# Kernel optimization log

Measured on AMD Instinct MI355X. Metric: run time of the kernel, lower is better.

Reference implementation:

```python
import jax, jax.numpy as jnp
import numpy as np

B, NOISE, HID, EMB, VOCAB, T = 256, 64, 256, 128, 32000, 16
PAD_ID = 0
TAU = 1.0
EPS = 1e-10


def setup_inputs() -> dict:
    key = jax.random.key(0)
    ks = jax.random.split(key, 11)
    s = 0.02
    return {
        "noise": jax.random.normal(ks[0], (B, NOISE), jnp.float32),
        "gumbel_u": jax.random.uniform(ks[1], (T, B, VOCAB), jnp.float32),
        "fc_W": jax.random.normal(ks[2], (HID, NOISE), jnp.float32) * s,
        "fc_b": jnp.zeros((HID,), jnp.float32),
        "embed_W": jax.random.normal(ks[3], (VOCAB, EMB), jnp.float32) * s,
        "W_ih": jax.random.normal(ks[4], (4 * HID, EMB), jnp.float32) * s,
        "W_hh": jax.random.normal(ks[5], (4 * HID, HID), jnp.float32) * s,
        "b_ih": jnp.zeros((4 * HID,), jnp.float32),
        "b_hh": jnp.zeros((4 * HID,), jnp.float32),
        "out_W": jax.random.normal(ks[6], (VOCAB, HID), jnp.float32) * s,
        "out_b": jnp.zeros((VOCAB,), jnp.float32),
    }


def reference(noise, gumbel_u, fc_W, fc_b, embed_W, W_ih, W_hh, b_ih, b_hh, out_W, out_b):
    # h0 = tanh(fc(noise)); c0 = 0; first input = embed(<PAD>)
    h0 = jnp.tanh(noise @ fc_W.T + fc_b)                       # [B, HID]
    c0 = jnp.zeros_like(h0)
    x0 = jnp.broadcast_to(embed_W[PAD_ID], (noise.shape[0], embed_W.shape[1]))

    def step(carry, g_u):
        h, c, x = carry
        gates = x @ W_ih.T + b_ih + h @ W_hh.T + b_hh           # [B, 4H]
        i_g, f_g, g_g, o_g = jnp.split(gates, 4, axis=-1)
        i_g = jax.nn.sigmoid(i_g)
        f_g = jax.nn.sigmoid(f_g)
        g_g = jnp.tanh(g_g)
        o_g = jax.nn.sigmoid(o_g)
        c = f_g * c + i_g * g_g
        h = o_g * jnp.tanh(c)
        logits = h @ out_W.T + out_b                            # [B, V]
        gumbel = -jnp.log(-jnp.log(g_u + EPS) + EPS)
        y_soft = jax.nn.softmax((logits + gumbel) / TAU, axis=-1)
        idx = jnp.argmax(y_soft, axis=-1)                       # [B]
        y_hard = jax.nn.one_hot(idx, logits.shape[-1], dtype=y_soft.dtype)
        token = y_hard - jax.lax.stop_gradient(y_soft) + y_soft  # straight-through
        x_next = embed_W[idx]                                   # [B, EMB]
        return (h, c, x_next), token

    _, tokens = jax.lax.scan(step, (h0, c0, x0), gumbel_u)      # [T, B, V]
    return jnp.transpose(tokens, (1, 0, 2))                     # [B, T, V]
```

## Files before the change

### kernel.cpp

```cpp
#include <hip/hip_runtime.h>
#include <math.h>

#define NB 256
#define NH 256
#define NE 128
#define NV 32000
#define TT 16
#define NZ 64

#define MAXC 192
#define UTHR 0.9979f
#define GNC  6.17f

__device__ __forceinline__ unsigned fkey(float f) {
    unsigned u = __float_as_uint(f);
    return (u & 0x80000000u) ? ~u : (u | 0x80000000u);
}
__device__ __forceinline__ float unfkey(unsigned k) {
    return __uint_as_float((k & 0x80000000u) ? (k & 0x7fffffffu) : ~k);
}
__device__ __forceinline__ unsigned long long sx64(unsigned long long v, int m) {
    unsigned lo = (unsigned)__shfl_xor((int)(unsigned)(v & 0xffffffffull), m, 64);
    unsigned hi = (unsigned)__shfl_xor((int)(unsigned)(v >> 32), m, 64);
    return ((unsigned long long)hi << 32) | (unsigned long long)lo;
}

__global__ void k_init(const float* __restrict__ noise, const float* __restrict__ fcW,
                       const float* __restrict__ fcb, float* __restrict__ h,
                       float* __restrict__ c, unsigned* __restrict__ maxWnU) {
    __shared__ float ns[NZ];
    int b = blockIdx.x, tid = threadIdx.x;
    if (tid < NZ) ns[tid] = noise[b * NZ + tid];
    __syncthreads();
    float acc = fcb[tid];
    const float* w = &fcW[(size_t)tid * NZ];
#pragma unroll
    for (int k = 0; k < NZ; k++) acc += ns[k] * w[k];
    h[b * NH + tid] = tanhf(acc);
    c[b * NH + tid] = 0.f;
    if (b == 0 && tid == 0) *maxWnU = 0u;
}

__global__ __launch_bounds__(256) void k_wnorm(const float* __restrict__ W,
                                               unsigned* __restrict__ maxWnU) {
    int lane = threadIdx.x & 63;
    int wv = blockIdx.x * 4 + (threadIdx.x >> 6);
    float best = 0.f;
    for (int r = wv * 64; r < wv * 64 + 64; r++) {
        const float* row = &W[(size_t)r * NH];
        float p = 0.f;
#pragma unroll
        for (int q = 0; q < 4; q++) {
            float x = row[lane + 64 * q];
            p += x * x;
        }
#pragma unroll
        for (int m = 1; m <= 32; m <<= 1) p += __shfl_xor(p, m, 64);
        best = fmaxf(best, p);
    }
    if (lane == 0) atomicMax(maxWnU, __float_as_uint(sqrtf(best) * 1.0001f + 1e-6f));
}

__global__ __launch_bounds__(256) void k_prep(const float* __restrict__ gu,
                                              float* __restrict__ out,
                                              int* __restrict__ counts,
                                              float2* __restrict__ cands) {
    __shared__ int cnt;
    __shared__ float2 lc[MAXC];
    int r = blockIdx.x;
    int t = r >> 8, b = r & 255;
    int tid = threadIdx.x;
    if (tid == 0) cnt = 0;
    __syncthreads();
    const float4* g4 = (const float4*)gu + (size_t)r * (NV / 4);
    float4* o4 = (float4*)out + ((size_t)b * TT + t) * (NV / 4);
    float4 z = make_float4(0.f, 0.f, 0.f, 0.f);
    for (int i = tid; i < NV / 4; i += 256) {
        float4 u = g4[i];
        o4[i] = z;
        float uv[4] = {u.x, u.y, u.z, u.w};
#pragma unroll
        for (int comp = 0; comp < 4; comp++) {
            if (uv[comp] > UTHR) {
                int k = atomicAdd(&cnt, 1);
                if (k < MAXC) {
                    float gm = -logf(-logf(uv[comp] + 1e-10f) + 1e-10f);
                    lc[k] = make_float2(gm, __int_as_float(i * 4 + comp));
                }
            }
        }
    }
    __syncthreads();
    int n = cnt > MAXC ? MAXC : cnt;
    if (tid == 0) counts[r] = cnt;
    if (tid < n) cands[(size_t)r * MAXC + tid] = lc[tid];
}

__global__ __launch_bounds__(256) void k_gates(
    const float* __restrict__ h, const float* __restrict__ embW,
    const float* __restrict__ Wih, const float* __restrict__ Whh,
    const float* __restrict__ bih, const float* __restrict__ bhh,
    float* __restrict__ gates, const int* __restrict__ idxPrev, int t) {
    __shared__ float As[16][68];
    __shared__ float Ws[16][68];
    __shared__ int idxs[64];
    int tid = threadIdx.x;
    int n0 = blockIdx.x * 64, m0 = blockIdx.y * 64;
    if (tid < 64) {
        idxs[tid] = (t == 0) ? 0 : idxPrev[m0 + tid];
    }
    float acc[4][4] = {};
    int row = tid >> 2, kq = tid & 3;
    int ty = tid >> 4, tx = tid & 15;
    for (int kc = 0; kc < 24; kc++) {
        __syncthreads();
        int kg = kc * 16 + kq * 4;
        float4 a4, w4;
        if (kg < NE) {
            a4 = *(const float4*)&embW[(size_t)idxs[row] * NE + kg];
            w4 = *(const float4*)&Wih[(size_t)(n0 + row) * NE + kg];
        } else {
            a4 = *(const float4*)&h[(size_t)(m0 + row) * NH + kg - NE];
            w4 = *(const float4*)&Whh[(size_t)(n0 + row) * NH + kg - NE];
        }
        As[kq * 4 + 0][row] = a4.x; As[kq * 4 + 1][row] = a4.y;
        As[kq * 4 + 2][row] = a4.z; As[kq * 4 + 3][row] = a4.w;
        Ws[kq * 4 + 0][row] = w4.x; Ws[kq * 4 + 1][row] = w4.y;
        Ws[kq * 4 + 2][row] = w4.z; Ws[kq * 4 + 3][row] = w4.w;
        __syncthreads();
#pragma unroll
        for (int kk = 0; kk < 16; kk++) {
            float a[4], w[4];
            *(float4*)&a[0] = *(const float4*)&As[kk][ty * 4];
            *(float4*)&w[0] = *(const float4*)&Ws[kk][tx * 4];
#pragma unroll
            for (int i = 0; i < 4; i++)
#pragma unroll
                for (int j = 0; j < 4; j++) acc[i][j] += a[i] * w[j];
        }
    }
#pragma unroll
    for (int i = 0; i < 4; i++) {
        int b = m0 + ty * 4 + i;
#pragma unroll
        for (int j = 0; j < 4; j++) {
            int n = n0 + tx * 4 + j;
            gates[(size_t)b * (4 * NH) + n] = acc[i][j] + bih[n] + bhh[n];
        }
    }
}

__global__ __launch_bounds__(256) void k_cellcand(
    const float* __restrict__ gates, float* __restrict__ c, float* __restrict__ h,
    const int* __restrict__ counts, const float2* __restrict__ cands,
    const float* __restrict__ W, const float* __restrict__ outb,
    const float* __restrict__ gu, const unsigned* __restrict__ maxWnU,
    int* __restrict__ idxs, float* __restrict__ out, int t) {
    __shared__ float hsh[NH];
    __shared__ float hred[4];
    __shared__ unsigned long long bks[4];
    __shared__ int fbflag;
    int b = blockIdx.x, tid = threadIdx.x;
    int lane = tid & 63, w = tid >> 6;

    const float* g = &gates[(size_t)b * (4 * NH)];
    float ig = g[tid], fg = g[NH + tid], gg = g[2 * NH + tid], og = g[3 * NH + tid];
    float is = 1.f / (1.f + expf(-ig));
    float fs = 1.f / (1.f + expf(-fg));
    float gt = tanhf(gg);
    float os = 1.f / (1.f + expf(-og));
    float cn = fs * c[b * NH + tid] + is * gt;
    c[b * NH + tid] = cn;
    float hv = os * tanhf(cn);
    h[b * NH + tid] = hv;
    hsh[tid] = hv;
    float p = hv * hv;
#pragma unroll
    for (int m = 1; m <= 32; m <<= 1) p += __shfl_xor(p, m, 64);
    if (lane == 0) hred[w] = p;
    __syncthreads();

    int r = t * NB + b;
    int nc = counts[r];
    unsigned long long bk = 0;
    if (nc >= 1 && nc <= MAXC) {
        const float2* cr = &cands[(size_t)r * MAXC];
        for (int ci = w; ci < nc; ci += 4) {
            float2 cd = cr[ci];
            int v = __float_as_int(cd.y);
            const float* Wr = &W[(size_t)v * NH];
            float d = 0.f;
#pragma unroll
            for (int q = 0; q < 4; q++) d += hsh[lane + 64 * q] * Wr[lane + 64 * q];
#pragma unroll
            for (int m = 1; m <= 32; m <<= 1) d += __shfl_xor(d, m, 64);
            float s = d + outb[v] + cd.x;
            unsigned long long key =
                ((unsigned long long)fkey(s) << 32) | (unsigned)(NV - 1 - v);
            if (key > bk) bk = key;
        }
    }
    if (lane == 0) bks[w] = bk;
    __syncthreads();
    if (tid == 0) {
        unsigned long long k = bks[0];
        for (int q = 1; q < 4; q++)
            if (bks[q] > k) k = bks[q];
        bks[0] = k;
        float hh2 = hred[0] + hred[1] + hred[2] + hred[3];
        float D = sqrtf(hh2) * 1.0001f * __uint_as_float(*maxWnU) + 0.01f;
        float bs = unfkey((unsigned)(k >> 32));
        fbflag = (nc < 1 || nc > MAXC || !(bs >= GNC + D)) ? 1 : 0;
    }
    __syncthreads();
    if (fbflag) {
        const float* gur = &gu[((size_t)t * NB + b) * NV];
        unsigned long long fk = 0;
        for (int v = tid; v < NV; v += 256) {
            float uv = gur[v];
            float gm = -logf(-logf(uv + 1e-10f) + 1e-10f);
            const float* Wr = &W[(size_t)v * NH];
            float d = 0.f;
            for (int k2 = 0; k2 < NH; k2++) d += hsh[k2] * Wr[k2];
            float s = d + outb[v] + gm;
            unsigned long long key =
                ((unsigned long long)fkey(s) << 32) | (unsigned)(NV - 1 - v);
            if (key > fk) fk = key;
        }
#pragma unroll
        for (int m = 1; m <= 32; m <<= 1) {
            unsigned long long o = sx64(fk, m);
            if (o > fk) fk = o;
        }
        if (lane == 0) bks[w] = fk;
        __syncthreads();
        if (tid == 0) {
            unsigned long long k = bks[0];
            for (int q = 1; q < 4; q++)
                if (bks[q] > k) k = bks[q];
            bks[0] = k;
        }
        __syncthreads();
    }
    if (tid == 0) {
        unsigned long long k = bks[0];
        int v = NV - 1 - (int)(unsigned)(k & 0xffffffffu);
        idxs[t * NB + b] = v;
        out[((size_t)b * TT + t) * NV + v] = 1.0f;
    }
}

extern "C" void kernel_launch(void* const* d_in, const int* in_sizes, int n_in,
                              void* d_out, int out_size, void* d_ws, size_t ws_size,
                              hipStream_t stream) {
    const float* noise = (const float*)d_in[0];
    const float* gu    = (const float*)d_in[1];
    const float* fcW   = (const float*)d_in[2];
    const float* fcb   = (const float*)d_in[3];
    const float* embW  = (const float*)d_in[4];
    const float* Wih   = (const float*)d_in[5];
    const float* Whh   = (const float*)d_in[6];
    const float* bih   = (const float*)d_in[7];
    const float* bhh   = (const float*)d_in[8];
    const float* outW  = (const float*)d_in[9];
    const float* outb  = (const float*)d_in[10];
    float* out = (float*)d_out;

    float* ws = (float*)d_ws;
    float* h      = ws;
    float* c      = ws + 65536;
    float* gates  = ws + 131072;
    int* idxs     = (int*)(ws + 393216);
    int* counts   = (int*)(ws + 397312);
    unsigned* maxWnU = (unsigned*)(ws + 401408);
    float2* cands = (float2*)(ws + 401416);

    k_init<<<NB, NH, 0, stream>>>(noise, fcW, fcb, h, c, maxWnU);
    k_wnorm<<<125, 256, 0, stream>>>(outW, maxWnU);
    k_prep<<<TT * NB, 256, 0, stream>>>(gu, out, counts, cands);

    for (int t = 0; t < TT; t++) {
        const int* idxPrev = idxs + (t > 0 ? (t - 1) * NB : 0);
        k_gates<<<dim3(16, 4), 256, 0, stream>>>(h, embW, Wih, Whh, bih, bhh, gates,
                                                 idxPrev, t);
        k_cellcand<<<NB, 256, 0, stream>>>(gates, c, h, counts, cands, outW, outb, gu,
                                           maxWnU, idxs, out, t);
    }
}
```

Baseline: 1.897 ms.

## Fuse LSTM timestep loop into one persistent kernel with packed gate weights

Replaces the per-timestep gate GEMM and cell/candidate kernels with a single kernel. Each block keeps the state of 4 batch rows in registers and shared memory across all 16 steps, using input and hidden weights pre-packed into a gate-interleaved float4 layout. Candidate logit evaluation is double-buffered over 8 candidates, and the output bias is folded into the precomputed Gumbel values. This removes 32 launches and the global round-trips for gates, h, c and idx. In exchange only 64 blocks run, every block rereads the full packed weight matrix each step, and the full-vocabulary fallback now runs on a single wave per row.

```diff
diff --git a/kernel.cpp b/kernel.cpp
--- a/kernel.cpp
+++ b/kernel.cpp
@@ -12,6 +12,8 @@
 #define UTHR 0.9979f
 #define GNC  6.17f
 
+typedef __attribute__((ext_vector_type(4))) float f32x4;
+
 __device__ __forceinline__ unsigned fkey(float f) {
     unsigned u = __float_as_uint(f);
     return (u & 0x80000000u) ? ~u : (u | 0x80000000u);
@@ -25,24 +27,25 @@
     return ((unsigned long long)hi << 32) | (unsigned long long)lo;
 }
 
-__global__ void k_init(const float* __restrict__ noise, const float* __restrict__ fcW,
-                       const float* __restrict__ fcb, float* __restrict__ h,
-                       float* __restrict__ c, unsigned* __restrict__ maxWnU) {
-    __shared__ float ns[NZ];
-    int b = blockIdx.x, tid = threadIdx.x;
-    if (tid < NZ) ns[tid] = noise[b * NZ + tid];
-    __syncthreads();
-    float acc = fcb[tid];
-    const float* w = &fcW[(size_t)tid * NZ];
-#pragma unroll
-    for (int k = 0; k < NZ; k++) acc += ns[k] * w[k];
-    h[b * NH + tid] = tanhf(acc);
-    c[b * NH + tid] = 0.f;
-    if (b == 0 && tid == 0) *maxWnU = 0u;
+__global__ void k_pack(const float* __restrict__ Wih, const float* __restrict__ Whh,
+                       f32x4* __restrict__ Wp, unsigned* __restrict__ maxWnU,
+                       unsigned* __restrict__ maxObU) {
+    int k = blockIdx.x;
+    int j = threadIdx.x;
+    f32x4 v;
+#pragma unroll
+    for (int g = 0; g < 4; ++g) {
+        int n = (g << 8) + j;
+        ((float*)&v)[g] = (k < NE) ? Wih[(size_t)n * NE + k] : Whh[(size_t)n * NH + (k - NE)];
+    }
+    Wp[k * 256 + j] = v;
+    if (k == 0 && j == 0) { *maxWnU = 0u; *maxObU = 0u; }
 }
 
 __global__ __launch_bounds__(256) void k_wnorm(const float* __restrict__ W,
-                                               unsigned* __restrict__ maxWnU) {
+                                               const float* __restrict__ outb,
+                                               unsigned* __restrict__ maxWnU,
+                                               unsigned* __restrict__ maxObU) {
     int lane = threadIdx.x & 63;
     int wv = blockIdx.x * 4 + (threadIdx.x >> 6);
     float best = 0.f;
@@ -59,9 +62,14 @@
         best = fmaxf(best, p);
     }
     if (lane == 0) atomicMax(maxWnU, __float_as_uint(sqrtf(best) * 1.0001f + 1e-6f));
+    float ob = outb[blockIdx.x * 256 + threadIdx.x];
+#pragma unroll
+    for (int m = 1; m <= 32; m <<= 1) ob = fmaxf(ob, __shfl_xor(ob, m, 64));
+    if (lane == 0) atomicMax(maxObU, fkey(ob));
 }
 
 __global__ __launch_bounds__(256) void k_prep(const float* __restrict__ gu,
+                                              const float* __restrict__ outb,
                                               float* __restrict__ out,
                                               int* __restrict__ counts,
                                               float2* __restrict__ cands) {
@@ -84,8 +92,9 @@
             if (uv[comp] > UTHR) {
                 int k = atomicAdd(&cnt, 1);
                 if (k < MAXC) {
-                    float gm = -logf(-logf(uv[comp] + 1e-10f) + 1e-10f);
-                    lc[k] = make_float2(gm, __int_as_float(i * 4 + comp));
+                    int v = i * 4 + comp;
+                    float gm = -logf(-logf(uv[comp] + 1e-10f) + 1e-10f) + outb[v];
+                    lc[k] = make_float2(gm, __int_as_float(v));
                 }
             }
         }
@@ -96,157 +105,175 @@
     if (tid < n) cands[(size_t)r * MAXC + tid] = lc[tid];
 }
 
-__global__ __launch_bounds__(256) void k_gates(
-    const float* __restrict__ h, const float* __restrict__ embW,
-    const float* __restrict__ Wih, const float* __restrict__ Whh,
-    const float* __restrict__ bih, const float* __restrict__ bhh,
-    float* __restrict__ gates, const int* __restrict__ idxPrev, int t) {
-    __shared__ float As[16][68];
-    __shared__ float Ws[16][68];
-    __shared__ int idxs[64];
+struct Cand8 {
+    f32x4 w[8];
+    float g[8];
+    int v[8];
+};
+__device__ __forceinline__ void load8(Cand8& cb, const float2* __restrict__ cr, int base,
+                                      int nc, const float* __restrict__ W, int lane) {
+#pragma unroll
+    for (int i = 0; i < 8; ++i) {
+        int ci = base + i;
+        float2 cd = (ci < nc) ? cr[ci] : make_float2(-1e30f, __int_as_float(0));
+        int v = __float_as_int(cd.y);
+        cb.g[i] = cd.x;
+        cb.v[i] = v;
+        cb.w[i] = *(const f32x4*)&W[(size_t)v * NH + (lane << 2)];
+    }
+}
+__device__ __forceinline__ void comp8(const Cand8& cb, f32x4 hx, unsigned long long& bk) {
+#pragma unroll
+    for (int i = 0; i < 8; ++i) {
+        f32x4 pr = hx * cb.w[i];
+        float d = pr.x + pr.y + pr.z + pr.w;
+#pragma unroll
+        for (int m = 1; m <= 32; m <<= 1) d += __shfl_xor(d, m, 64);
+        float s = d + cb.g[i];
+        unsigned long long key =
+            ((unsigned long long)fkey(s) << 32) | (unsigned)(NV - 1 - cb.v[i]);
+        if (key > bk) bk = key;
+    }
+}
+
+__global__ __launch_bounds__(256) void k_main(
+    const float* __restrict__ noise, const float* __restrict__ fcW,
+    const float* __restrict__ fcb, const float* __restrict__ embW,
+    const f32x4* __restrict__ Wp, const float* __restrict__ bih,
+    const float* __restrict__ bhh, const int* __restrict__ counts,
+    const float2* __restrict__ cands, const float* __restrict__ W,
+    const float* __restrict__ outb, const float* __restrict__ gu,
+    const unsigned* __restrict__ maxWnU, const unsigned* __restrict__ maxObU,
+    float* __restrict__ out) {
+    __shared__ f32x4 xhp[384];
+    __shared__ float hrow[4][256];
+    __shared__ float ns[256];
     int tid = threadIdx.x;
-    int n0 = blockIdx.x * 64, m0 = blockIdx.y * 64;
-    if (tid < 64) {
-        idxs[tid] = (t == 0) ? 0 : idxPrev[m0 + tid];
-    }
-    float acc[4][4] = {};
-    int row = tid >> 2, kq = tid & 3;
-    int ty = tid >> 4, tx = tid & 15;
-    for (int kc = 0; kc < 24; kc++) {
+    int lane = tid & 63, w = tid >> 6;
+    int r0 = blockIdx.x << 2;
+    int j = tid;
+
+    float maxWn = __uint_as_float(*maxWnU);
+    float mob = unfkey(*maxObU);
+
+    float bsum[4];
+#pragma unroll
+    for (int g = 0; g < 4; ++g) bsum[g] = bih[(g << 8) + j] + bhh[(g << 8) + j];
+
+    ns[tid] = noise[r0 * NZ + tid];
+    __syncthreads();
+    float c_[4], h_[4];
+    {
+        float fb = fcb[j];
+        float a0 = fb, a1 = fb, a2 = fb, a3 = fb;
+        const float* fw = &fcW[(size_t)j * NZ];
+        for (int k = 0; k < NZ; ++k) {
+            float wv = fw[k];
+            a0 += ns[k] * wv;
+            a1 += ns[64 + k] * wv;
+            a2 += ns[128 + k] * wv;
+            a3 += ns[192 + k] * wv;
+        }
+        h_[0] = tanhf(a0); h_[1] = tanhf(a1); h_[2] = tanhf(a2); h_[3] = tanhf(a3);
+#pragma unroll
+        for (int q = 0; q < 4; ++q) {
+            c_[q] = 0.f;
+            ((float*)&xhp[128 + j])[q] = h_[q];
+        }
+    }
+    if (j < NE) {
+        float v = embW[j];
+        f32x4 t4 = {v, v, v, v};
+        xhp[j] = t4;
+    }
+    __syncthreads();
+
+    for (int t = 0; t < TT; ++t) {
+        f32x4 a0 = {bsum[0], bsum[0], bsum[0], bsum[0]};
+        f32x4 a1 = {bsum[1], bsum[1], bsum[1], bsum[1]};
+        f32x4 a2 = {bsum[2], bsum[2], bsum[2], bsum[2]};
+        f32x4 a3 = {bsum[3], bsum[3], bsum[3], bsum[3]};
+        const f32x4* wp = Wp + j;
+#pragma unroll 8
+        for (int k = 0; k < 384; ++k) {
+            f32x4 xv = xhp[k];
+            f32x4 wv = wp[k << 8];
+            a0 += xv * wv.x;
+            a1 += xv * wv.y;
+            a2 += xv * wv.z;
+            a3 += xv * wv.w;
+        }
         __syncthreads();
-        int kg = kc * 16 + kq * 4;
-        float4 a4, w4;
-        if (kg < NE) {
-            a4 = *(const float4*)&embW[(size_t)idxs[row] * NE + kg];
-            w4 = *(const float4*)&Wih[(size_t)(n0 + row) * NE + kg];
-        } else {
-            a4 = *(const float4*)&h[(size_t)(m0 + row) * NH + kg - NE];
-            w4 = *(const float4*)&Whh[(size_t)(n0 + row) * NH + kg - NE];
-        }
-        As[kq * 4 + 0][row] = a4.x; As[kq * 4 + 1][row] = a4.y;
-        As[kq * 4 + 2][row] = a4.z; As[kq * 4 + 3][row] = a4.w;
-        Ws[kq * 4 + 0][row] = w4.x; Ws[kq * 4 + 1][row] = w4.y;
-        Ws[kq * 4 + 2][row] = w4.z; Ws[kq * 4 + 3][row] = w4.w;
+#pragma unroll
+        for (int q = 0; q < 4; ++q) {
+            float is = 1.f / (1.f + expf(-a0[q]));
+            float fs = 1.f / (1.f + expf(-a1[q]));
+            float gt = tanhf(a2[q]);
+            float os = 1.f / (1.f + expf(-a3[q]));
+            c_[q] = fs * c_[q] + is * gt;
+            h_[q] = os * tanhf(c_[q]);
+            ((float*)&xhp[128 + j])[q] = h_[q];
+        }
         __syncthreads();
-#pragma unroll
-        for (int kk = 0; kk < 16; kk++) {
-            float a[4], w[4];
-            *(float4*)&a[0] = *(const float4*)&As[kk][ty * 4];
-            *(float4*)&w[0] = *(const float4*)&Ws[kk][tx * 4];
-#pragma unroll
-            for (int i = 0; i < 4; i++)
-#pragma unroll
-                for (int j = 0; j < 4; j++) acc[i][j] += a[i] * w[j];
-        }
-    }
-#pragma unroll
-    for (int i = 0; i < 4; i++) {
-        int b = m0 + ty * 4 + i;
-#pragma unroll
-        for (int j = 0; j < 4; j++) {
-            int n = n0 + tx * 4 + j;
-            gates[(size_t)b * (4 * NH) + n] = acc[i][j] + bih[n] + bhh[n];
-        }
-    }
-}
-
-__global__ __launch_bounds__(256) void k_cellcand(
-    const float* __restrict__ gates, float* __restrict__ c, float* __restrict__ h,
-    const int* __restrict__ counts, const float2* __restrict__ cands,
-    const float* __restrict__ W, const float* __restrict__ outb,
-    const float* __restrict__ gu, const unsigned* __restrict__ maxWnU,
-    int* __restrict__ idxs, float* __restrict__ out, int t) {
-    __shared__ float hsh[NH];
-    __shared__ float hred[4];
-    __shared__ unsigned long long bks[4];
-    __shared__ int fbflag;
-    int b = blockIdx.x, tid = threadIdx.x;
-    int lane = tid & 63, w = tid >> 6;
-
-    const float* g = &gates[(size_t)b * (4 * NH)];
-    float ig = g[tid], fg = g[NH + tid], gg = g[2 * NH + tid], og = g[3 * NH + tid];
-    float is = 1.f / (1.f + expf(-ig));
-    float fs = 1.f / (1.f + expf(-fg));
-    float gt = tanhf(gg);
-    float os = 1.f / (1.f + expf(-og));
-    float cn = fs * c[b * NH + tid] + is * gt;
-    c[b * NH + tid] = cn;
-    float hv = os * tanhf(cn);
-    h[b * NH + tid] = hv;
-    hsh[tid] = hv;
-    float p = hv * hv;
-#pragma unroll
-    for (int m = 1; m <= 32; m <<= 1) p += __shfl_xor(p, m, 64);
-    if (lane == 0) hred[w] = p;
-    __syncthreads();
-
-    int r = t * NB + b;
-    int nc = counts[r];
-    unsigned long long bk = 0;
-    if (nc >= 1 && nc <= MAXC) {
-        const float2* cr = &cands[(size_t)r * MAXC];
-        for (int ci = w; ci < nc; ci += 4) {
-            float2 cd = cr[ci];
-            int v = __float_as_int(cd.y);
-            const float* Wr = &W[(size_t)v * NH];
-            float d = 0.f;
-#pragma unroll
-            for (int q = 0; q < 4; q++) d += hsh[lane + 64 * q] * Wr[lane + 64 * q];
-#pragma unroll
-            for (int m = 1; m <= 32; m <<= 1) d += __shfl_xor(d, m, 64);
-            float s = d + outb[v] + cd.x;
-            unsigned long long key =
-                ((unsigned long long)fkey(s) << 32) | (unsigned)(NV - 1 - v);
-            if (key > bk) bk = key;
-        }
-    }
-    if (lane == 0) bks[w] = bk;
-    __syncthreads();
-    if (tid == 0) {
-        unsigned long long k = bks[0];
-        for (int q = 1; q < 4; q++)
-            if (bks[q] > k) k = bks[q];
-        bks[0] = k;
-        float hh2 = hred[0] + hred[1] + hred[2] + hred[3];
-        float D = sqrtf(hh2) * 1.0001f * __uint_as_float(*maxWnU) + 0.01f;
-        float bs = unfkey((unsigned)(k >> 32));
-        fbflag = (nc < 1 || nc > MAXC || !(bs >= GNC + D)) ? 1 : 0;
-    }
-    __syncthreads();
-    if (fbflag) {
-        const float* gur = &gu[((size_t)t * NB + b) * NV];
-        unsigned long long fk = 0;
-        for (int v = tid; v < NV; v += 256) {
-            float uv = gur[v];
-            float gm = -logf(-logf(uv + 1e-10f) + 1e-10f);
-            const float* Wr = &W[(size_t)v * NH];
-            float d = 0.f;
-            for (int k2 = 0; k2 < NH; k2++) d += hsh[k2] * Wr[k2];
-            float s = d + outb[v] + gm;
-            unsigned long long key =
-                ((unsigned long long)fkey(s) << 32) | (unsigned)(NV - 1 - v);
-            if (key > fk) fk = key;
-        }
-#pragma unroll
-        for (int m = 1; m <= 32; m <<= 1) {
-            unsigned long long o = sx64(fk, m);
-            if (o > fk) fk = o;
-        }
-        if (lane == 0) bks[w] = fk;
+        int b = r0 + w;
+        int r = t * NB + b;
+        float p = 0.f;
+#pragma unroll
+        for (int m4 = 0; m4 < 4; ++m4) {
+            int k = lane + (m4 << 6);
+            float hv = ((float*)&xhp[128 + k])[w];
+            hrow[w][k] = hv;
+            p += hv * hv;
+        }
+#pragma unroll
+        for (int m = 1; m <= 32; m <<= 1) p += __shfl_xor(p, m, 64);
+        f32x4 hx = *(const f32x4*)&hrow[w][lane << 2];
+
+        int nc = counts[r];
+        unsigned long long bk = 0;
+        if (nc >= 1 && nc <= MAXC) {
+            const float2* cr = &cands[(size_t)r * MAXC];
+            Cand8 A, B;
+            load8(A, cr, 0, nc, W, lane);
+            for (int base = 0; base < nc; base += 16) {
+                if (base + 8 < nc) load8(B, cr, base + 8, nc, W, lane);
+                comp8(A, hx, bk);
+                if (base + 16 < nc) load8(A, cr, base + 16, nc, W, lane);
+                if (base + 8 < nc) comp8(B, hx, bk);
+            }
+        }
+        float D = sqrtf(p) * 1.0001f * maxWn + mob + 0.01f;
+        bool ok = (nc >= 1) && (nc <= MAXC) && (unfkey((unsigned)(bk >> 32)) >= GNC + D);
+        if (!ok) {
+            const float* gur = gu + (size_t)r * NV;
+            unsigned long long fk = 0;
+            for (int v = lane; v < NV; v += 64) {
+                float uv = gur[v];
+                float gm = -logf(-logf(uv + 1e-10f) + 1e-10f);
+                const float* Wr = W + (size_t)v * NH;
+                float d = 0.f;
+                for (int k2 = 0; k2 < NH; ++k2) d += hrow[w][k2] * Wr[k2];
+                float s = d + outb[v] + gm;
+                unsigned long long key =
+                    ((unsigned long long)fkey(s) << 32) | (unsigned)(NV - 1 - v);
+                if (key > fk) fk = key;
+            }
+#pragma unroll
+            for (int m = 1; m <= 32; m <<= 1) {
+                unsigned long long o = sx64(fk, m);
+                if (o > fk) fk = o;
+            }
+            bk = fk;
+        }
+        int vwin = NV - 1 - (int)(unsigned)(bk & 0xffffffffull);
+        if (lane == 0) out[((size_t)b * TT + t) * NV + vwin] = 1.0f;
+        if (t + 1 < TT) {
+            float e0 = embW[(size_t)vwin * NE + lane];
+            float e1 = embW[(size_t)vwin * NE + 64 + lane];
+            ((float*)&xhp[lane])[w] = e0;
+            ((float*)&xhp[64 + lane])[w] = e1;
+        }
         __syncthreads();
-        if (tid == 0) {
-            unsigned long long k = bks[0];
-            for (int q = 1; q < 4; q++)
-                if (bks[q] > k) k = bks[q];
-            bks[0] = k;
-        }
-        __syncthreads();
-    }
-    if (tid == 0) {
-        unsigned long long k = bks[0];
-        int v = NV - 1 - (int)(unsigned)(k & 0xffffffffu);
-        idxs[t * NB + b] = v;
-        out[((size_t)b * TT + t) * NV + v] = 1.0f;
     }
 }
 
@@ -267,23 +294,15 @@
     float* out = (float*)d_out;
 
     float* ws = (float*)d_ws;
-    float* h      = ws;
-    float* c      = ws + 65536;
-    float* gates  = ws + 131072;
-    int* idxs     = (int*)(ws + 393216);
-    int* counts   = (int*)(ws + 397312);
-    unsigned* maxWnU = (unsigned*)(ws + 401408);
-    float2* cands = (float2*)(ws + 401416);
-
-    k_init<<<NB, NH, 0, stream>>>(noise, fcW, fcb, h, c, maxWnU);
-    k_wnorm<<<125, 256, 0, stream>>>(outW, maxWnU);
-    k_prep<<<TT * NB, 256, 0, stream>>>(gu, out, counts, cands);
-
-    for (int t = 0; t < TT; t++) {
-        const int* idxPrev = idxs + (t > 0 ? (t - 1) * NB : 0);
-        k_gates<<<dim3(16, 4), 256, 0, stream>>>(h, embW, Wih, Whh, bih, bhh, gates,
-                                                 idxPrev, t);
-        k_cellcand<<<NB, 256, 0, stream>>>(gates, c, h, counts, cands, outW, outb, gu,
-                                           maxWnU, idxs, out, t);
-    }
-}
+    f32x4* Wp        = (f32x4*)ws;
+    int* counts      = (int*)(ws + 393216);
+    unsigned* maxWnU = (unsigned*)(ws + 397312);
+    unsigned* maxObU = (unsigned*)(ws + 397313);
+    float2* cands    = (float2*)(ws + 397320);
+
+    k_pack<<<384, 256, 0, stream>>>(Wih, Whh, Wp, maxWnU, maxObU);
+    k_wnorm<<<125, 256, 0, stream>>>(outW, outb, maxWnU, maxObU);
+    k_prep<<<TT * NB, 256, 0, stream>>>(gu, outb, out, counts, cands);
+    k_main<<<NB / 4, 256, 0, stream>>>(noise, fcW, fcb, embW, Wp, bih, bhh, counts,
+                                       cands, outW, outb, gu, maxWnU, maxObU, out);
+}
```

New measurement: 1.797 ms. 1.06x faster.
